# Performance work log

Hardware: AMD Instinct MI355X
Metric: run time of the kernel (lower is better)

Reference implementation:

```python
import jax, jax.numpy as jnp
import numpy as np
from jax.scipy.special import logsumexp

COST_GAMMA = 0.1
MIN_ZERO_GAMMA = 0.1
_CLIP = 1.0 - 1e-7


def setup_inputs() -> dict:
    key = jax.random.key(0)
    k1, k2, k3 = jax.random.split(key, 3)
    B, D, K = 65536, 128, 1024
    xs = jax.random.normal(k1, (B, D), dtype=jnp.float32)
    xs = xs / jnp.linalg.norm(xs, axis=-1, keepdims=True)  # points on sphere S^{D-1}
    mus = jax.random.normal(k2, (D, K), dtype=jnp.float32)  # prototype params (pre-projx)
    alphas = jax.random.uniform(k3, (K,), dtype=jnp.float32)
    return {"xs": xs, "mus": mus, "alphas": alphas}


def reference(xs, mus, alphas):
    # projx: project prototype columns onto the unit sphere
    mus_p = mus / jnp.linalg.norm(mus, axis=0, keepdims=True)  # [D, K]
    # sphere cost: half squared geodesic distance, cdist-like [B, K]
    ip = jnp.clip(xs @ mus_p, -_CLIP, _CLIP)
    costs = 0.5 * jnp.arccos(ip) ** 2 + alphas  # [B, K]
    # softmin over components via stable logsumexp
    F = COST_GAMMA * logsumexp(-costs / COST_GAMMA, axis=1)  # [B]
    # soft min(F, 0): logsumexp over stacked (F, 0) == logaddexp
    F = MIN_ZERO_GAMMA * jnp.logaddexp(-F / MIN_ZERO_GAMMA, 0.0)
    return F
```

## Files before the change

kernel.cpp:

```cpp
#include <hip/hip_runtime.h>
#include <hip/hip_bf16.h>


typedef __attribute__((ext_vector_type(8))) short short8;
typedef __attribute__((ext_vector_type(4))) float f32x4;
typedef __attribute__((ext_vector_type(2))) float f32x2;

#define KP 1024
#define DD 128

__device__ __forceinline__ unsigned int f2bf(float f) {
  unsigned int u = __float_as_uint(f);
  return (u + 0x7FFFu + ((u >> 16) & 1u)) >> 16;
}

__device__ __forceinline__ f32x2 pk_fma(f32x2 a, f32x2 b, f32x2 c) {
  return __builtin_elementwise_fma(a, b, c);
}

__global__ __launch_bounds__(256) void prep_kernel(
    const float* __restrict__ mus, const float* __restrict__ alphas,
    uint4* __restrict__ musbf_sw, float* __restrict__ lw) {
  __shared__ float psum[8][32];
  __shared__ float Tt[32][129];
  __shared__ float inv_s[32];
  const int t = threadIdx.x;
  const int k0 = blockIdx.x * 32;
  const int kk = t & 31, gg = t >> 5;
  float s = 0.0f;
  for (int i = 0; i < 16; ++i) {
    float v = mus[(gg * 16 + i) * KP + k0 + kk];
    s = fmaf(v, v, s);
  }
  psum[gg][kk] = s;
  __syncthreads();
  if (t < 32) {
    float tot = 0.0f;
    for (int j = 0; j < 8; ++j) tot += psum[j][t];
    inv_s[t] = rsqrtf(tot);
    lw[k0 + t] = -14.4269504089f * alphas[k0 + t];
  }
  for (int i = 0; i < 16; ++i) {
    int e = i * 256 + t;
    Tt[e & 31][e >> 5] = mus[(e >> 5) * KP + k0 + (e & 31)];
  }
  __syncthreads();
  #pragma unroll
  for (int i = 0; i < 2; ++i) {
    int u = i * 256 + t;
    int w0 = u >> 5, c32 = u & 31;
    int col = k0 + c32;
    float inv = inv_s[c32];
    uint4 o;
    o.x = f2bf(Tt[c32][w0 * 8 + 0] * inv) | (f2bf(Tt[c32][w0 * 8 + 1] * inv) << 16);
    o.y = f2bf(Tt[c32][w0 * 8 + 2] * inv) | (f2bf(Tt[c32][w0 * 8 + 3] * inv) << 16);
    o.z = f2bf(Tt[c32][w0 * 8 + 4] * inv) | (f2bf(Tt[c32][w0 * 8 + 5] * inv) << 16);
    o.w = f2bf(Tt[c32][w0 * 8 + 6] * inv) | (f2bf(Tt[c32][w0 * 8 + 7] * inv) << 16);
    musbf_sw[((col >> 6) << 10) + (w0 << 6) + (col & 63)] = o;
  }
}

__global__ __launch_bounds__(128, 2) void main_kernel(
    const float* __restrict__ xs, const uint4* __restrict__ musbf_sw,
    const float* __restrict__ lw, float* __restrict__ out) {
  __shared__ __align__(16) unsigned short Bs[2][8192];
  const int t = threadIdx.x;
  const int wv = t >> 6, ln = t & 63, q = ln >> 4, l15 = ln & 15;

  const int row0 = blockIdx.x * 64 + wv * 32 + l15;
  const float4* xs4 = (const float4*)xs;
  short8 afr[2][4];
  #pragma unroll
  for (int rt = 0; rt < 2; ++rt) {
    const int base4 = (row0 + rt * 16) * 32 + q * 2;
    #pragma unroll
    for (int kkk = 0; kkk < 4; ++kkk) {
      float4 f0 = xs4[base4 + kkk * 8];
      float4 f1 = xs4[base4 + kkk * 8 + 1];
      union { short8 s; uint4 u; } a;
      a.u.x = f2bf(f0.x) | (f2bf(f0.y) << 16);
      a.u.y = f2bf(f0.z) | (f2bf(f0.w) << 16);
      a.u.z = f2bf(f1.x) | (f2bf(f1.y) << 16);
      a.u.w = f2bf(f1.z) | (f2bf(f1.w) << 16);
      afr[rt][kkk] = a.s;
    }
  }

  uint4 v[8];
  #pragma unroll
  for (int i = 0; i < 8; ++i) v[i] = musbf_sw[i * 128 + t];
  #pragma unroll
  for (int i = 0; i < 8; ++i) *(uint4*)&Bs[0][(i * 128 + t) * 8] = v[i];
  __syncthreads();

  const f32x2 C_mh = {-0.5f, -0.5f}, C_ph = {0.5f, 0.5f};
  const f32x2 C_z0 = {0.0f, 0.0f};
  const f32x2 C5 = {-3.6067376f, -3.6067376f};
  const f32x2 C4 = {-2.3449500f, -2.3449500f};
  const f32x2 C3 = {-3.2975886f, -3.2975886f};
  const f32x2 C2 = {-5.1295823f, -5.1295823f};
  const f32x2 C1 = {-9.6179669f, -9.6179669f};
  const f32x2 C0 = {-28.8539008f, -28.8539008f};

  f32x2 sums2[2][2] = {{(f32x2){0.f, 0.f}, (f32x2){0.f, 0.f}},
                       {(f32x2){0.f, 0.f}, (f32x2){0.f, 0.f}}};

  for (int cg = 0; cg < 16; ++cg) {
    if (cg < 15) {
      #pragma unroll
      for (int i = 0; i < 8; ++i)
        v[i] = musbf_sw[(cg + 1) * 1024 + i * 128 + t];
    }
    float lwv[4];
    #pragma unroll
    for (int nt = 0; nt < 4; ++nt) lwv[nt] = lw[cg * 64 + nt * 16 + l15];

    f32x4 acc[2][4];
    #pragma unroll
    for (int rt = 0; rt < 2; ++rt)
      #pragma unroll
      for (int nt = 0; nt < 4; ++nt) acc[rt][nt] = (f32x4){0.f, 0.f, 0.f, 0.f};

    const unsigned short* bp = &Bs[cg & 1][q * 512 + l15 * 8];
    #pragma unroll
    for (int kkk = 0; kkk < 4; ++kkk)
      #pragma unroll
      for (int nt = 0; nt < 4; ++nt) {
        short8 b = *(const short8*)(bp + kkk * 2048 + nt * 128);
        acc[0][nt] = __builtin_amdgcn_mfma_f32_16x16x32_bf16(afr[0][kkk], b, acc[0][nt], 0, 0, 0);
        acc[1][nt] = __builtin_amdgcn_mfma_f32_16x16x32_bf16(afr[1][kkk], b, acc[1][nt], 0, 0, 0);
      }

    #pragma unroll
    for (int rt = 0; rt < 2; ++rt)
      #pragma unroll
      for (int nt = 0; nt < 4; ++nt) {
        f32x2 lwp = {lwv[nt], lwv[nt]};
        #pragma unroll
        for (int p = 0; p < 2; ++p) {
          f32x2 x = {acc[rt][nt][2 * p], acc[rt][nt][2 * p + 1]};
          f32x2 z = pk_fma(x, C_mh, C_ph);
          z = __builtin_elementwise_max(z, C_z0);
          f32x2 h = pk_fma(z, C5, C4);
          h = pk_fma(z, h, C3);
          h = pk_fma(z, h, C2);
          h = pk_fma(z, h, C1);
          h = pk_fma(z, h, C0);
          f32x2 arg = pk_fma(z, h, lwp);
          f32x2 e = {__builtin_amdgcn_exp2f(arg.x), __builtin_amdgcn_exp2f(arg.y)};
          sums2[rt][p] = sums2[rt][p] + e;
        }
      }

    if (cg < 15) {
      #pragma unroll
      for (int i = 0; i < 8; ++i)
        *(uint4*)&Bs[(cg + 1) & 1][(i * 128 + t) * 8] = v[i];
      __syncthreads();
    }
  }

  #pragma unroll
  for (int rt = 0; rt < 2; ++rt) {
    float s[4] = {sums2[rt][0].x, sums2[rt][0].y, sums2[rt][1].x, sums2[rt][1].y};
    #pragma unroll
    for (int s2 = 1; s2 < 16; s2 <<= 1)
      #pragma unroll
      for (int r = 0; r < 4; ++r) s[r] += __shfl_xor(s[r], s2, 64);
    if (l15 == 0) {
      #pragma unroll
      for (int r = 0; r < 4; ++r)
        out[blockIdx.x * 64 + wv * 32 + rt * 16 + q * 4 + r] =
            0.1f * log1pf(1.0f / s[r]);
    }
  }
}

extern "C" void kernel_launch(void* const* d_in, const int* in_sizes, int n_in,
                              void* d_out, int out_size, void* d_ws, size_t ws_size,
                              hipStream_t stream) {
  const float* xs     = (const float*)d_in[0];
  const float* mus    = (const float*)d_in[1];
  const float* alphas = (const float*)d_in[2];
  float* out = (float*)d_out;

  uint4* musbf_sw = (uint4*)d_ws;
  float* lw = (float*)((char*)d_ws + 16384 * sizeof(uint4));

  prep_kernel<<<KP / 32, 256, 0, stream>>>(mus, alphas, musbf_sw, lw);
  const int B = in_sizes[0] / DD;
  main_kernel<<<B / 64, 128, 0, stream>>>(xs, musbf_sw, lw, out);
}
```

Measured before the change: 108.4 us.

## Load B fragments directly from global into registers, drop LDS staging

Removes the shared-memory double buffer and barriers for the prototype tile. Each wave now loads its MFMA B operands straight from global memory (L2/L1-resident) into two register buffers, ping-ponging between them. Blocks grow to 256 threads with 128 rows each. This removes LDS writes, reads and __syncthreads, but raises VGPR pressure (32 short8 registers) and repeats the global/L1 traffic once per wave instead of once per block.

```diff
diff --git a/kernel.cpp b/kernel.cpp
--- a/kernel.cpp
+++ b/kernel.cpp
@@ -60,14 +60,13 @@
   }
 }
 
-__global__ __launch_bounds__(128, 2) void main_kernel(
+__global__ __launch_bounds__(256, 2) void main_kernel(
     const float* __restrict__ xs, const uint4* __restrict__ musbf_sw,
     const float* __restrict__ lw, float* __restrict__ out) {
-  __shared__ __align__(16) unsigned short Bs[2][8192];
   const int t = threadIdx.x;
   const int wv = t >> 6, ln = t & 63, q = ln >> 4, l15 = ln & 15;
 
-  const int row0 = blockIdx.x * 64 + wv * 32 + l15;
+  const int row0 = blockIdx.x * 128 + wv * 32 + l15;
   const float4* xs4 = (const float4*)xs;
   short8 afr[2][4];
   #pragma unroll
@@ -86,13 +85,6 @@
     }
   }
 
-  uint4 v[8];
-  #pragma unroll
-  for (int i = 0; i < 8; ++i) v[i] = musbf_sw[i * 128 + t];
-  #pragma unroll
-  for (int i = 0; i < 8; ++i) *(uint4*)&Bs[0][(i * 128 + t) * 8] = v[i];
-  __syncthreads();
-
   const f32x2 C_mh = {-0.5f, -0.5f}, C_ph = {0.5f, 0.5f};
   const f32x2 C_z0 = {0.0f, 0.0f};
   const f32x2 C5 = {-3.6067376f, -3.6067376f};
@@ -105,12 +97,10 @@
   f32x2 sums2[2][2] = {{(f32x2){0.f, 0.f}, (f32x2){0.f, 0.f}},
                        {(f32x2){0.f, 0.f}, (f32x2){0.f, 0.f}}};
 
-  for (int cg = 0; cg < 16; ++cg) {
-    if (cg < 15) {
-      #pragma unroll
-      for (int i = 0; i < 8; ++i)
-        v[i] = musbf_sw[(cg + 1) * 1024 + i * 128 + t];
-    }
+  const short8* __restrict__ B8 = (const short8*)musbf_sw;
+  const int ub = q * 64 + l15;
+
+  auto compute = [&](int cg, const short8* bv) {
     float lwv[4];
     #pragma unroll
     for (int nt = 0; nt < 4; ++nt) lwv[nt] = lw[cg * 64 + nt * 16 + l15];
@@ -121,12 +111,11 @@
       #pragma unroll
       for (int nt = 0; nt < 4; ++nt) acc[rt][nt] = (f32x4){0.f, 0.f, 0.f, 0.f};
 
-    const unsigned short* bp = &Bs[cg & 1][q * 512 + l15 * 8];
     #pragma unroll
     for (int kkk = 0; kkk < 4; ++kkk)
       #pragma unroll
       for (int nt = 0; nt < 4; ++nt) {
-        short8 b = *(const short8*)(bp + kkk * 2048 + nt * 128);
+        short8 b = bv[kkk * 4 + nt];
         acc[0][nt] = __builtin_amdgcn_mfma_f32_16x16x32_bf16(afr[0][kkk], b, acc[0][nt], 0, 0, 0);
         acc[1][nt] = __builtin_amdgcn_mfma_f32_16x16x32_bf16(afr[1][kkk], b, acc[1][nt], 0, 0, 0);
       }
@@ -151,13 +140,24 @@
           sums2[rt][p] = sums2[rt][p] + e;
         }
       }
+  };
 
-    if (cg < 15) {
+  short8 b0[16], b1[16];
+  #pragma unroll
+  for (int j = 0; j < 16; ++j)
+    b0[j] = B8[(j >> 2) * 256 + (j & 3) * 16 + ub];
+
+  for (int cg = 0; cg < 16; cg += 2) {
+    #pragma unroll
+    for (int j = 0; j < 16; ++j)
+      b1[j] = B8[(cg + 1) * 1024 + (j >> 2) * 256 + (j & 3) * 16 + ub];
+    compute(cg, b0);
+    if (cg < 14) {
       #pragma unroll
-      for (int i = 0; i < 8; ++i)
-        *(uint4*)&Bs[(cg + 1) & 1][(i * 128 + t) * 8] = v[i];
-      __syncthreads();
+      for (int j = 0; j < 16; ++j)
+        b0[j] = B8[(cg + 2) * 1024 + (j >> 2) * 256 + (j & 3) * 16 + ub];
     }
+    compute(cg + 1, b1);
   }
 
   #pragma unroll
@@ -170,7 +170,7 @@
     if (l15 == 0) {
       #pragma unroll
       for (int r = 0; r < 4; ++r)
-        out[blockIdx.x * 64 + wv * 32 + rt * 16 + q * 4 + r] =
+        out[blockIdx.x * 128 + wv * 32 + rt * 16 + q * 4 + r] =
             0.1f * log1pf(1.0f / s[r]);
     }
   }
@@ -189,5 +189,5 @@
 
   prep_kernel<<<KP / 32, 256, 0, stream>>>(mus, alphas, musbf_sw, lw);
   const int B = in_sizes[0] / DD;
-  main_kernel<<<B / 64, 128, 0, stream>>>(xs, musbf_sw, lw, out);
+  main_kernel<<<B / 128, 256, 0, stream>>>(xs, musbf_sw, lw, out);
 }
```

New measurement: 109.6 us. Within noise of the previous version (+1.1%).
